# Performance work log

Measured on AMD Instinct MI355X. Metric: run time of the kernel, lower is better.

## Reference

```python
import jax, jax.numpy as jnp
import numpy as np

NEG_INF = -1e30


def setup_inputs() -> dict:
    key = jax.random.key(0)
    ks = jax.random.split(key, 8)
    B, N, I, O, H = 8, 1024, 64, 32, 4
    return {
        "x": jax.random.normal(ks[0], (B, N, I), dtype=jnp.float32),
        "adj": jax.random.randint(ks[1], (N, N), 0, 2, dtype=jnp.int32),
        "source_prior": jax.random.normal(ks[2], (B, N), dtype=jnp.float32),
        "beta": jax.random.normal(ks[3], (H,), dtype=jnp.float32),
        "weight": jax.random.normal(ks[4], (H, I, O), dtype=jnp.float32) * (1.0 / np.sqrt(I)),
        "attn_src": jax.random.normal(ks[5], (H, O), dtype=jnp.float32) * (1.0 / np.sqrt(O)),
        "attn_dst": jax.random.normal(ks[6], (H, O), dtype=jnp.float32) * (1.0 / np.sqrt(O)),
        "bias": jnp.zeros((H, O), dtype=jnp.float32),
    }


def reference(x, adj, source_prior, beta, weight, attn_src, attn_dst, bias):
    B, N, _ = x.shape
    H, _, O = weight.shape
    # Per-head projection + bias: [B,H,N,O]
    projected = jnp.einsum('bni,hio->bhno', x, weight) + bias[None, :, None, :]
    src_scores = jnp.einsum('bhnd,hd->bhn', projected, attn_src)  # [B,H,N]
    dst_scores = jnp.einsum('bhnd,hd->bhn', projected, attn_dst)  # [B,H,N]
    # Additive attention logits: [B,H,dst,src]
    logits = jax.nn.leaky_relu(dst_scores[..., :, None] + src_scores[..., None, :],
                               negative_slope=0.2)
    # Source-prior correction
    gain = jax.nn.softplus(beta).reshape(1, H, 1, 1)
    logits = logits + gain * source_prior[:, None, None, :]
    # Masked softmax over sources; fully-masked rows stay zero
    mask = (adj != 0)[None, None, :, :]  # [1,1,N,N]
    masked = jnp.where(mask, logits, NEG_INF)
    row_max = jnp.max(masked, axis=-1, keepdims=True)
    row_max = jnp.where(jnp.isfinite(row_max) & (row_max > NEG_INF / 2),
                        row_max, jnp.zeros_like(row_max))
    exp_logits = jnp.where(mask, jnp.exp(logits - row_max), 0.0)
    eps = jnp.finfo(logits.dtype).eps
    denom = jnp.maximum(jnp.sum(exp_logits, axis=-1, keepdims=True), eps)
    attention = exp_logits / denom  # [B,H,N,N]
    # Weighted aggregation: [B,H,N,O]
    output = jnp.einsum('bhij,bhjd->bhid', attention, projected)
    # concat=True: [B,N,H*O]
    encoded = jnp.transpose(output, (0, 2, 1, 3)).reshape(B, N, H * O)
    return encoded
```

## Files before the change

kernel.cpp:

```cpp
#include <hip/hip_runtime.h>
#include <math.h>

#define NB 8
#define NN 1024
#define NI 64
#define NO 32
#define NH 4
#define NEGINF (-1e30f)

typedef _Float16 half8 __attribute__((ext_vector_type(8)));
typedef _Float16 half4v __attribute__((ext_vector_type(4)));
typedef float floatx4 __attribute__((ext_vector_type(4)));

__global__ __launch_bounds__(256) void k_pack(const int* __restrict__ adj,
                                              unsigned char* __restrict__ adjb) {
    const int i = blockIdx.x * 256 + threadIdx.x;
    const int4 v = ((const int4*)adj)[i];
    unsigned int p = (v.x ? 1u : 0u) | ((v.y ? 1u : 0u) << 8) |
                     ((v.z ? 1u : 0u) << 16) | ((v.w ? 1u : 0u) << 24);
    ((unsigned int*)adjb)[i] = p;
}

__global__ __launch_bounds__(256) void k_proj(
    const float* __restrict__ x, const float* __restrict__ beta,
    const float* __restrict__ weight, const float* __restrict__ attn_src,
    const float* __restrict__ attn_dst, const float* __restrict__ bias,
    const float* __restrict__ prior,
    _Float16* __restrict__ projT,
    float* __restrict__ src_s, float* __restrict__ dst_s, float* __restrict__ gp)
{
    __shared__ __align__(16) float xs[32 * 64];
    __shared__ __align__(16) float ws[4 * 64 * 36];
    const int t = threadIdx.x;
    const int ntile = blockIdx.x, b = blockIdx.y;
    const int n0b = ntile * 32;
    {
        const float4* xsrc = (const float4*)(x + ((size_t)b * NN + n0b) * NI);
        float4* xd = (float4*)xs;
        xd[t] = xsrc[t];
        xd[t + 256] = xsrc[t + 256];
    }
    #pragma unroll
    for (int k = 0; k < 8; ++k) {
        int e = t + k * 256;
        int h = e >> 9, rem = e & 511, i = rem >> 3, o4 = rem & 7;
        float4 wv = *(const float4*)(weight + (h * NI + i) * NO + o4 * 4);
        *(float4*)&ws[h * 2304 + i * 36 + o4 * 4] = wv;
    }
    __syncthreads();

    const int o4 = t & 7, h = (t >> 3) & 3, ng = t >> 5;
    const int o0 = o4 * 4, nl0 = ng * 4;
    float acc[4][4];
    #pragma unroll
    for (int kn = 0; kn < 4; ++kn)
        #pragma unroll
        for (int oo = 0; oo < 4; ++oo) acc[kn][oo] = 0.f;

    #pragma unroll 4
    for (int i = 0; i < NI; ++i) {
        const float4 wv = *(const float4*)&ws[h * 2304 + i * 36 + o0];
        #pragma unroll
        for (int kn = 0; kn < 4; ++kn) {
            const float xv = xs[(nl0 + kn) * 64 + i];
            acc[kn][0] = fmaf(xv, wv.x, acc[kn][0]);
            acc[kn][1] = fmaf(xv, wv.y, acc[kn][1]);
            acc[kn][2] = fmaf(xv, wv.z, acc[kn][2]);
            acc[kn][3] = fmaf(xv, wv.w, acc[kn][3]);
        }
    }
    const float4 bv  = *(const float4*)(bias + h * NO + o0);
    const float4 asv = *(const float4*)(attn_src + h * NO + o0);
    const float4 adv = *(const float4*)(attn_dst + h * NO + o0);
    const int bh = b * NH + h;
    float ssum[4], dsum[4];
    #pragma unroll
    for (int kn = 0; kn < 4; ++kn) {
        acc[kn][0] += bv.x; acc[kn][1] += bv.y;
        acc[kn][2] += bv.z; acc[kn][3] += bv.w;
        ssum[kn] = acc[kn][0]*asv.x + acc[kn][1]*asv.y + acc[kn][2]*asv.z + acc[kn][3]*asv.w;
        dsum[kn] = acc[kn][0]*adv.x + acc[kn][1]*adv.y + acc[kn][2]*adv.z + acc[kn][3]*adv.w;
    }
    #pragma unroll
    for (int oo = 0; oo < 4; ++oo) {
        half4v hv;
        hv[0] = (_Float16)acc[0][oo]; hv[1] = (_Float16)acc[1][oo];
        hv[2] = (_Float16)acc[2][oo]; hv[3] = (_Float16)acc[3][oo];
        *(half4v*)(projT + ((size_t)(bh * NO + o0 + oo)) * NN + n0b + nl0) = hv;
    }
    #pragma unroll
    for (int msk = 1; msk <= 4; msk <<= 1) {
        #pragma unroll
        for (int kn = 0; kn < 4; ++kn) {
            ssum[kn] += __shfl_xor(ssum[kn], msk, 64);
            dsum[kn] += __shfl_xor(dsum[kn], msk, 64);
        }
    }
    if (o4 == 0) {
        const float bx = beta[h];
        const float sp = fmaxf(bx, 0.f) + log1pf(__expf(-fabsf(bx)));
        #pragma unroll
        for (int kn = 0; kn < 4; ++kn) {
            const int n = n0b + nl0 + kn;
            src_s[bh * NN + n] = ssum[kn];
            dst_s[bh * NN + n] = dsum[kn];
            gp[bh * NN + n] = sp * prior[b * NN + n];
        }
    }
}

#define VTP 1032

__global__ __launch_bounds__(256) void k_attn(
    const unsigned char* __restrict__ adjb,
    const _Float16* __restrict__ projT,
    const float* __restrict__ src_s, const float* __restrict__ dst_s,
    const float* __restrict__ gp,
    float* __restrict__ out)
{
    __shared__ __align__(16) _Float16 vt[NO * VTP];
    __shared__ __align__(16) float srcs[NN];
    __shared__ __align__(16) float gps[NN];
    __shared__ float pmax[64 * 4];
    const int t = threadIdx.x;
    const int lane = t & 63, wave = t >> 6;
    const int dtile = blockIdx.x, h = blockIdx.y, b = blockIdx.z;
    const int bh = b * NH + h;

    ((float4*)srcs)[t] = ((const float4*)(src_s + bh * NN))[t];
    ((float4*)gps)[t]  = ((const float4*)(gp + bh * NN))[t];
    const _Float16* ptrow = projT + (size_t)bh * NO * NN;
    #pragma unroll
    for (int k = 0; k < 16; ++k) {
        const int e = t + k * 256;
        const int o = e >> 7, sc8 = e & 127;
        *(half8*)&vt[o * VTP + sc8 * 8] =
            *(const half8*)(ptrow + (size_t)o * NN + sc8 * 8);
    }
    __syncthreads();

    {
        const int dl = lane, qt = wave;
        const int drow = dtile * 64 + dl;
        const float dv = dst_s[bh * NN + drow];
        const unsigned char* ar = adjb + (size_t)drow * NN + qt * 256;
        float mx = NEGINF;
        #pragma unroll 4
        for (int k = 0; k < 16; ++k) {
            const uint4 a4 = *(const uint4*)(ar + k * 16);
            const unsigned int wv[4] = {a4.x, a4.y, a4.z, a4.w};
            const int sb = qt * 256 + k * 16;
            #pragma unroll
            for (int w = 0; w < 4; ++w) {
                #pragma unroll
                for (int byi = 0; byi < 4; ++byi) {
                    const int s = sb + w * 4 + byi;
                    const float ts = dv + srcs[s];
                    const float sc = fmaxf(ts, 0.f) + 0.2f * fminf(ts, 0.f) + gps[s];
                    const bool on = (wv[w] >> (8 * byi)) & 1;
                    mx = fmaxf(mx, on ? sc : NEGINF);
                }
            }
        }
        pmax[dl * 4 + qt] = mx;
    }
    __syncthreads();

    const int m = lane & 15, quad = lane >> 4;
    const int d = dtile * 64 + wave * 16 + m;
    const float dreg = dst_s[bh * NN + d];
    const int pmb = (wave * 16 + m) * 4;
    const float rmx = fmaxf(fmaxf(pmax[pmb], pmax[pmb + 1]),
                            fmaxf(pmax[pmb + 2], pmax[pmb + 3]));
    const float rmc = (rmx > -1e29f) ? rmx : 0.f;
    const unsigned char* adjr = adjb + (size_t)d * NN;

    floatx4 acc0 = {0.f, 0.f, 0.f, 0.f}, acc1 = {0.f, 0.f, 0.f, 0.f};
    float psum = 0.f;
    uint2 apre = *(const uint2*)(adjr + quad * 8);

    for (int st = 0; st < 32; ++st) {
        const uint2 acur = apre;
        if (st < 31) apre = *(const uint2*)(adjr + (st + 1) * 32 + quad * 8);
        const int sg = st * 32 + quad * 8;
        float sv[8], gv[8];
        *(float4*)&sv[0] = *(const float4*)&srcs[sg];
        *(float4*)&sv[4] = *(const float4*)&srcs[sg + 4];
        *(float4*)&gv[0] = *(const float4*)&gps[sg];
        *(float4*)&gv[4] = *(const float4*)&gps[sg + 4];
        half8 af;
        #pragma unroll
        for (int j = 0; j < 8; ++j) {
            const unsigned int bit =
                ((j < 4 ? (acur.x >> (8 * j)) : (acur.y >> (8 * (j - 4)))) & 1u);
            const float ts = dreg + sv[j];
            const float lk = fmaxf(ts, 0.f) + 0.2f * fminf(ts, 0.f);
            const float sce = bit ? (lk + gv[j]) : NEGINF;
            const float p = __expf(sce - rmc);
            psum += p;
            af[j] = (_Float16)p;
        }
        const half8 b0 = *(const half8*)&vt[m * VTP + sg];
        const half8 b1 = *(const half8*)&vt[(16 + m) * VTP + sg];
        acc0 = __builtin_amdgcn_mfma_f32_16x16x32_f16(af, b0, acc0, 0, 0, 0);
        acc1 = __builtin_amdgcn_mfma_f32_16x16x32_f16(af, b1, acc1, 0, 0, 0);
    }
    psum += __shfl_xor(psum, 16, 64);
    psum += __shfl_xor(psum, 32, 64);

    #pragma unroll
    for (int r = 0; r < 4; ++r) {
        const int row = quad * 4 + r;
        const float lr = __shfl(psum, row, 64);
        const float inv = 1.f / fmaxf(lr, 1.1920929e-07f);
        float* go = out + ((size_t)(b * NN + dtile * 64 + wave * 16 + row)) * (NH * NO) + h * NO;
        go[m] = acc0[r] * inv;
        go[16 + m] = acc1[r] * inv;
    }
}

extern "C" void kernel_launch(void* const* d_in, const int* in_sizes, int n_in,
                              void* d_out, int out_size, void* d_ws, size_t ws_size,
                              hipStream_t stream) {
    (void)in_sizes; (void)n_in; (void)out_size; (void)ws_size;
    const float* x        = (const float*)d_in[0];
    const int*   adj      = (const int*)d_in[1];
    const float* prior    = (const float*)d_in[2];
    const float* beta     = (const float*)d_in[3];
    const float* weight   = (const float*)d_in[4];
    const float* attn_src = (const float*)d_in[5];
    const float* attn_dst = (const float*)d_in[6];
    const float* bias     = (const float*)d_in[7];
    float* out = (float*)d_out;

    _Float16* projT = (_Float16*)d_ws;
    float* src_s = (float*)((char*)d_ws + (1 << 21));
    float* dst_s = src_s + NB * NH * NN;
    float* gpb   = dst_s + NB * NH * NN;
    unsigned char* adjb = (unsigned char*)(gpb + NB * NH * NN);

    hipLaunchKernelGGL(k_pack, dim3(1024), dim3(256), 0, stream, adj, adjb);
    hipLaunchKernelGGL(k_proj, dim3(32, 8), dim3(256), 0, stream,
                       x, beta, weight, attn_src, attn_dst, bias, prior,
                       projT, src_s, dst_s, gpb);
    hipLaunchKernelGGL(k_attn, dim3(16, 4, 8), dim3(256), 0, stream,
                       adjb, projT, src_s, dst_s, gpb, out);
}
```

Baseline: 110.0 us.

## Fuse adjacency packing into projection, use bound max and split-K attention

The adjacency packing kernel is merged into the projection kernel, which removes one launch. The exact per-row masked max pass is replaced by an upper bound, leaky(dst+max src)+max gp, and the scores are pre-scaled by log2e so exp2 can be used. The attention kernel no longer stages the full V matrix in shared memory. Each block now handles 16 destination rows, its four waves split the source dimension, V is loaded directly from global memory with prefetch, and partial results are reduced through shared memory. The looser max bound risks fp16 underflow for rows whose true max is far below the bound, and the new grid runs four times as many blocks.

```diff
diff --git a/kernel.cpp b/kernel.cpp
--- a/kernel.cpp
+++ b/kernel.cpp
@@ -6,34 +6,34 @@
 #define NI 64
 #define NO 32
 #define NH 4
-#define NEGINF (-1e30f)
+#define LOG2E 1.4426950408889634f
 
 typedef _Float16 half8 __attribute__((ext_vector_type(8)));
-typedef _Float16 half4v __attribute__((ext_vector_type(4)));
+typedef _Float16 half2v __attribute__((ext_vector_type(2)));
 typedef float floatx4 __attribute__((ext_vector_type(4)));
 
-__global__ __launch_bounds__(256) void k_pack(const int* __restrict__ adj,
-                                              unsigned char* __restrict__ adjb) {
-    const int i = blockIdx.x * 256 + threadIdx.x;
-    const int4 v = ((const int4*)adj)[i];
-    unsigned int p = (v.x ? 1u : 0u) | ((v.y ? 1u : 0u) << 8) |
-                     ((v.z ? 1u : 0u) << 16) | ((v.w ? 1u : 0u) << 24);
-    ((unsigned int*)adjb)[i] = p;
-}
-
 __global__ __launch_bounds__(256) void k_proj(
-    const float* __restrict__ x, const float* __restrict__ beta,
+    const float* __restrict__ x, const int* __restrict__ adj,
+    const float* __restrict__ prior, const float* __restrict__ beta,
     const float* __restrict__ weight, const float* __restrict__ attn_src,
     const float* __restrict__ attn_dst, const float* __restrict__ bias,
-    const float* __restrict__ prior,
     _Float16* __restrict__ projT,
-    float* __restrict__ src_s, float* __restrict__ dst_s, float* __restrict__ gp)
+    float* __restrict__ src_s, float* __restrict__ dst_s, float* __restrict__ gp_,
+    unsigned char* __restrict__ adjb)
 {
     __shared__ __align__(16) float xs[32 * 64];
     __shared__ __align__(16) float ws[4 * 64 * 36];
     const int t = threadIdx.x;
     const int ntile = blockIdx.x, b = blockIdx.y;
     const int n0b = ntile * 32;
+    #pragma unroll
+    for (int k = 0; k < 4; ++k) {
+        const int g = (b * 32 + ntile) * 1024 + k * 256 + t;
+        const int4 v = ((const int4*)adj)[g];
+        ((unsigned int*)adjb)[g] =
+            (v.x ? 1u : 0u) | ((v.y ? 1u : 0u) << 8) |
+            ((v.z ? 1u : 0u) << 16) | ((v.w ? 1u : 0u) << 24);
+    }
     {
         const float4* xsrc = (const float4*)(x + ((size_t)b * NN + n0b) * NI);
         float4* xd = (float4*)xs;
@@ -42,10 +42,10 @@
     }
     #pragma unroll
     for (int k = 0; k < 8; ++k) {
-        int e = t + k * 256;
-        int h = e >> 9, rem = e & 511, i = rem >> 3, o4 = rem & 7;
-        float4 wv = *(const float4*)(weight + (h * NI + i) * NO + o4 * 4);
-        *(float4*)&ws[h * 2304 + i * 36 + o4 * 4] = wv;
+        const int e = t + k * 256;
+        const int h = e >> 9, rem = e & 511, i = rem >> 3, o4 = rem & 7;
+        *(float4*)&ws[h * 2304 + i * 36 + o4 * 4] =
+            *(const float4*)(weight + (h * NI + i) * NO + o4 * 4);
     }
     __syncthreads();
 
@@ -83,10 +83,12 @@
     }
     #pragma unroll
     for (int oo = 0; oo < 4; ++oo) {
-        half4v hv;
-        hv[0] = (_Float16)acc[0][oo]; hv[1] = (_Float16)acc[1][oo];
-        hv[2] = (_Float16)acc[2][oo]; hv[3] = (_Float16)acc[3][oo];
-        *(half4v*)(projT + ((size_t)(bh * NO + o0 + oo)) * NN + n0b + nl0) = hv;
+        half2v h0, h1;
+        h0[0] = (_Float16)acc[0][oo]; h0[1] = (_Float16)acc[1][oo];
+        h1[0] = (_Float16)acc[2][oo]; h1[1] = (_Float16)acc[3][oo];
+        _Float16* pp = projT + ((size_t)(bh * NO + o0 + oo)) * NN + n0b + nl0;
+        *(half2v*)pp = h0;
+        *(half2v*)(pp + 2) = h1;
     }
     #pragma unroll
     for (int msk = 1; msk <= 4; msk <<= 1) {
@@ -102,106 +104,92 @@
         #pragma unroll
         for (int kn = 0; kn < 4; ++kn) {
             const int n = n0b + nl0 + kn;
-            src_s[bh * NN + n] = ssum[kn];
-            dst_s[bh * NN + n] = dsum[kn];
-            gp[bh * NN + n] = sp * prior[b * NN + n];
+            src_s[bh * NN + n] = LOG2E * ssum[kn];
+            dst_s[bh * NN + n] = LOG2E * dsum[kn];
+            gp_[bh * NN + n]   = LOG2E * sp * prior[b * NN + n];
         }
     }
 }
 
-#define VTP 1032
-
-__global__ __launch_bounds__(256) void k_attn(
+__global__ __launch_bounds__(256, 4) void k_attn(
     const unsigned char* __restrict__ adjb,
     const _Float16* __restrict__ projT,
     const float* __restrict__ src_s, const float* __restrict__ dst_s,
-    const float* __restrict__ gp,
+    const float* __restrict__ gp_,
     float* __restrict__ out)
 {
-    __shared__ __align__(16) _Float16 vt[NO * VTP];
     __shared__ __align__(16) float srcs[NN];
     __shared__ __align__(16) float gps[NN];
-    __shared__ float pmax[64 * 4];
+    __shared__ float red[8];
+    __shared__ float part[4][16][33];
+    __shared__ float ps[4][16];
+
     const int t = threadIdx.x;
     const int lane = t & 63, wave = t >> 6;
-    const int dtile = blockIdx.x, h = blockIdx.y, b = blockIdx.z;
+    const int rowtile = blockIdx.x, h = blockIdx.y, b = blockIdx.z;
     const int bh = b * NH + h;
 
-    ((float4*)srcs)[t] = ((const float4*)(src_s + bh * NN))[t];
-    ((float4*)gps)[t]  = ((const float4*)(gp + bh * NN))[t];
-    const _Float16* ptrow = projT + (size_t)bh * NO * NN;
-    #pragma unroll
-    for (int k = 0; k < 16; ++k) {
-        const int e = t + k * 256;
-        const int o = e >> 7, sc8 = e & 127;
-        *(half8*)&vt[o * VTP + sc8 * 8] =
-            *(const half8*)(ptrow + (size_t)o * NN + sc8 * 8);
-    }
+    const float4 s4 = ((const float4*)(src_s + bh * NN))[t];
+    const float4 g4 = ((const float4*)(gp_ + bh * NN))[t];
+    ((float4*)srcs)[t] = s4;
+    ((float4*)gps)[t]  = g4;
+    float s_l = fmaxf(fmaxf(s4.x, s4.y), fmaxf(s4.z, s4.w));
+    float g_l = fmaxf(fmaxf(g4.x, g4.y), fmaxf(g4.z, g4.w));
+    #pragma unroll
+    for (int msk = 1; msk <= 32; msk <<= 1) {
+        s_l = fmaxf(s_l, __shfl_xor(s_l, msk, 64));
+        g_l = fmaxf(g_l, __shfl_xor(g_l, msk, 64));
+    }
+    if (lane == 0) { red[wave * 2] = s_l; red[wave * 2 + 1] = g_l; }
     __syncthreads();
-
-    {
-        const int dl = lane, qt = wave;
-        const int drow = dtile * 64 + dl;
-        const float dv = dst_s[bh * NN + drow];
-        const unsigned char* ar = adjb + (size_t)drow * NN + qt * 256;
-        float mx = NEGINF;
-        #pragma unroll 4
-        for (int k = 0; k < 16; ++k) {
-            const uint4 a4 = *(const uint4*)(ar + k * 16);
-            const unsigned int wv[4] = {a4.x, a4.y, a4.z, a4.w};
-            const int sb = qt * 256 + k * 16;
-            #pragma unroll
-            for (int w = 0; w < 4; ++w) {
-                #pragma unroll
-                for (int byi = 0; byi < 4; ++byi) {
-                    const int s = sb + w * 4 + byi;
-                    const float ts = dv + srcs[s];
-                    const float sc = fmaxf(ts, 0.f) + 0.2f * fminf(ts, 0.f) + gps[s];
-                    const bool on = (wv[w] >> (8 * byi)) & 1;
-                    mx = fmaxf(mx, on ? sc : NEGINF);
-                }
-            }
-        }
-        pmax[dl * 4 + qt] = mx;
-    }
-    __syncthreads();
+    const float S = fmaxf(fmaxf(red[0], red[2]), fmaxf(red[4], red[6]));
+    const float G = fmaxf(fmaxf(red[1], red[3]), fmaxf(red[5], red[7]));
 
     const int m = lane & 15, quad = lane >> 4;
-    const int d = dtile * 64 + wave * 16 + m;
-    const float dreg = dst_s[bh * NN + d];
-    const int pmb = (wave * 16 + m) * 4;
-    const float rmx = fmaxf(fmaxf(pmax[pmb], pmax[pmb + 1]),
-                            fmaxf(pmax[pmb + 2], pmax[pmb + 3]));
-    const float rmc = (rmx > -1e29f) ? rmx : 0.f;
+    const int d = rowtile * 16 + m;
+    const float dregl = dst_s[bh * NN + d];
+    const float rmcl = fmaxf(dregl + S, 0.f) + G;
     const unsigned char* adjr = adjb + (size_t)d * NN;
+    const _Float16* ptr0 = projT + (size_t)(bh * NO + m) * NN;
+    const _Float16* ptr1 = ptr0 + 16 * NN;
 
     floatx4 acc0 = {0.f, 0.f, 0.f, 0.f}, acc1 = {0.f, 0.f, 0.f, 0.f};
     float psum = 0.f;
-    uint2 apre = *(const uint2*)(adjr + quad * 8);
-
-    for (int st = 0; st < 32; ++st) {
-        const uint2 acur = apre;
-        if (st < 31) apre = *(const uint2*)(adjr + (st + 1) * 32 + quad * 8);
-        const int sg = st * 32 + quad * 8;
+    int sg = wave * 256 + quad * 8;
+    uint2  aa  = *(const uint2*)(adjr + sg);
+    half8  vb0 = *(const half8*)(ptr0 + sg);
+    half8  vb1 = *(const half8*)(ptr1 + sg);
+
+    #pragma unroll
+    for (int st = 0; st < 8; ++st) {
+        const uint2 ac = aa;
+        const half8 b0 = vb0, b1 = vb1;
+        const int sgc = sg;
+        if (st < 7) {
+            sg += 32;
+            aa  = *(const uint2*)(adjr + sg);
+            vb0 = *(const half8*)(ptr0 + sg);
+            vb1 = *(const half8*)(ptr1 + sg);
+        }
         float sv[8], gv[8];
-        *(float4*)&sv[0] = *(const float4*)&srcs[sg];
-        *(float4*)&sv[4] = *(const float4*)&srcs[sg + 4];
-        *(float4*)&gv[0] = *(const float4*)&gps[sg];
-        *(float4*)&gv[4] = *(const float4*)&gps[sg + 4];
-        half8 af;
+        *(float4*)&sv[0] = *(const float4*)&srcs[sgc];
+        *(float4*)&sv[4] = *(const float4*)&srcs[sgc + 4];
+        *(float4*)&gv[0] = *(const float4*)&gps[sgc];
+        *(float4*)&gv[4] = *(const float4*)&gps[sgc + 4];
+        float p[8];
         #pragma unroll
         for (int j = 0; j < 8; ++j) {
             const unsigned int bit =
-                ((j < 4 ? (acur.x >> (8 * j)) : (acur.y >> (8 * (j - 4)))) & 1u);
-            const float ts = dreg + sv[j];
-            const float lk = fmaxf(ts, 0.f) + 0.2f * fminf(ts, 0.f);
-            const float sce = bit ? (lk + gv[j]) : NEGINF;
-            const float p = __expf(sce - rmc);
-            psum += p;
-            af[j] = (_Float16)p;
-        }
-        const half8 b0 = *(const half8*)&vt[m * VTP + sg];
-        const half8 b1 = *(const half8*)&vt[(16 + m) * VTP + sg];
+                ((j < 4 ? (ac.x >> (8 * j)) : (ac.y >> (8 * (j - 4)))) & 1u);
+            const float ts = dregl + sv[j];
+            const float lk = fmaxf(ts, 0.2f * ts);
+            const float arg = bit ? (lk + gv[j] - rmcl) : -1e30f;
+            p[j] = exp2f(arg);
+            psum += p[j];
+        }
+        half8 af;
+        #pragma unroll
+        for (int j = 0; j < 8; ++j) af[j] = (_Float16)p[j];
         acc0 = __builtin_amdgcn_mfma_f32_16x16x32_f16(af, b0, acc0, 0, 0, 0);
         acc1 = __builtin_amdgcn_mfma_f32_16x16x32_f16(af, b1, acc1, 0, 0, 0);
     }
@@ -210,13 +198,22 @@
 
     #pragma unroll
     for (int r = 0; r < 4; ++r) {
-        const int row = quad * 4 + r;
-        const float lr = __shfl(psum, row, 64);
-        const float inv = 1.f / fmaxf(lr, 1.1920929e-07f);
-        float* go = out + ((size_t)(b * NN + dtile * 64 + wave * 16 + row)) * (NH * NO) + h * NO;
-        go[m] = acc0[r] * inv;
-        go[16 + m] = acc1[r] * inv;
-    }
+        part[wave][quad * 4 + r][m]      = acc0[r];
+        part[wave][quad * 4 + r][16 + m] = acc1[r];
+    }
+    if (quad == 0) ps[wave][m] = psum;
+    __syncthreads();
+
+    const int row = t >> 4, col = t & 15;
+    const float denom = ps[0][row] + ps[1][row] + ps[2][row] + ps[3][row];
+    const float inv = 1.f / fmaxf(denom, 1.1920929e-07f);
+    const float v0 = part[0][row][col] + part[1][row][col] +
+                     part[2][row][col] + part[3][row][col];
+    const float v1 = part[0][row][16 + col] + part[1][row][16 + col] +
+                     part[2][row][16 + col] + part[3][row][16 + col];
+    float* go = out + ((size_t)(b * NN + rowtile * 16 + row)) * (NH * NO) + h * NO;
+    go[col]      = v0 * inv;
+    go[16 + col] = v1 * inv;
 }
 
 extern "C" void kernel_launch(void* const* d_in, const int* in_sizes, int n_in,
@@ -239,10 +236,9 @@
     float* gpb   = dst_s + NB * NH * NN;
     unsigned char* adjb = (unsigned char*)(gpb + NB * NH * NN);
 
-    hipLaunchKernelGGL(k_pack, dim3(1024), dim3(256), 0, stream, adj, adjb);
     hipLaunchKernelGGL(k_proj, dim3(32, 8), dim3(256), 0, stream,
-                       x, beta, weight, attn_src, attn_dst, bias, prior,
-                       projT, src_s, dst_s, gpb);
-    hipLaunchKernelGGL(k_attn, dim3(16, 4, 8), dim3(256), 0, stream,
+                       x, adj, prior, beta, weight, attn_src, attn_dst, bias,
+                       projT, src_s, dst_s, gpb, adjb);
+    hipLaunchKernelGGL(k_attn, dim3(64, 4, 8), dim3(256), 0, stream,
                        adjb, projT, src_s, dst_s, gpb, out);
 }
```

Result: faster. 104.8 us (-4.7%).
